# Performance work log

Measured on AMD Instinct MI355X. Metric: run time of the kernel, lower is better.

The kernel has to match this reference:

```python
import jax, jax.numpy as jnp
import numpy as np

B, T, D, H = 2, 2048, 1024, 16
DH = D // H
EPS = 1e-5


def layer_norm(x, g, b):
    m = jnp.mean(x, axis=-1, keepdims=True)
    v = jnp.mean((x - m) ** 2, axis=-1, keepdims=True)
    return (x - m) * jax.lax.rsqrt(v + EPS) * g + b


def setup_inputs() -> dict:
    key = jax.random.key(0)
    ks = jax.random.split(key, 12)
    s = 0.02
    return {
        "x_refined": jax.random.normal(ks[0], (B, T, D), jnp.float32),
        "x_mem": jax.random.normal(ks[1], (B, T, D), jnp.float32),
        "ln_q_g": jnp.ones((D,), jnp.float32), "ln_q_b": jnp.zeros((D,), jnp.float32),
        "ln_kv_g": jnp.ones((D,), jnp.float32), "ln_kv_b": jnp.zeros((D,), jnp.float32),
        "Wq": jax.random.normal(ks[2], (D, D), jnp.float32) * s,
        "bq": jnp.zeros((D,), jnp.float32),
        "Wk": jax.random.normal(ks[3], (D, D), jnp.float32) * s,
        "bk": jnp.zeros((D,), jnp.float32),
        "Wv": jax.random.normal(ks[4], (D, D), jnp.float32) * s,
        "bv": jnp.zeros((D,), jnp.float32),
        "Wo": jax.random.normal(ks[5], (D, D), jnp.float32) * s,
        "bo": jnp.zeros((D,), jnp.float32),
        "ln_f_g": jnp.ones((D,), jnp.float32), "ln_f_b": jnp.zeros((D,), jnp.float32),
        "W1": jax.random.normal(ks[6], (D, 4 * D), jnp.float32) * s,
        "b1": jnp.zeros((4 * D,), jnp.float32),
        "W2": jax.random.normal(ks[7], (4 * D, D), jnp.float32) * s,
        "b2": jnp.zeros((D,), jnp.float32),
        "band": 24,
    }


def reference(x_refined, x_mem, ln_q_g, ln_q_b, ln_kv_g, ln_kv_b,
              Wq, bq, Wk, bk, Wv, bv, Wo, bo,
              ln_f_g, ln_f_b, W1, b1, W2, b2, band):
    Q = layer_norm(x_refined, ln_q_g, ln_q_b)   # (B,T,D)
    KV = layer_norm(x_mem, ln_kv_g, ln_kv_b)    # (B,T,D)

    # projections, split into heads: (B,H,T,DH)
    q = (Q @ Wq + bq).reshape(B, T, H, DH).transpose(0, 2, 1, 3)
    k = (KV @ Wk + bk).reshape(B, T, H, DH).transpose(0, 2, 1, 3)
    v = (KV @ Wv + bv).reshape(B, T, H, DH).transpose(0, 2, 1, 3)

    scores = jnp.einsum('bhtd,bhsd->bhts', q, k) / jnp.sqrt(jnp.float32(DH))
    # banded additive mask: |t - s| <= band allowed (same math as the Python loop)
    idx = jnp.arange(T)
    allowed = jnp.abs(idx[:, None] - idx[None, :]) <= band  # (T,T)
    scores = jnp.where(allowed[None, None], scores, -jnp.inf)
    attn = jax.nn.softmax(scores, axis=-1)

    ctx = jnp.einsum('bhts,bhsd->bhtd', attn, v)            # (B,H,T,DH)
    ctx = ctx.transpose(0, 2, 1, 3).reshape(B, T, D)
    y = x_refined + (ctx @ Wo + bo)

    h = layer_norm(y, ln_f_g, ln_f_b)
    h = jax.nn.gelu(h @ W1 + b1, approximate=False) @ W2 + b2
    return y + h
```

## Files before the change

kernel.cpp:

```cpp
#include <hip/hip_runtime.h>
#include <math.h>
#include <stdint.h>

#define TSEQ   2048
#define DMODEL 1024
#define NHEAD  16
#define DHEAD  64
#define MROWS  4096

typedef short bf16x8 __attribute__((ext_vector_type(8)));
typedef float f32x4  __attribute__((ext_vector_type(4)));
typedef unsigned short u16;

typedef __attribute__((address_space(3))) unsigned int lds_u32_t;
typedef __attribute__((address_space(1))) unsigned int glb_u32_t;

static __device__ __forceinline__ u16 f2bf(float f) {
    unsigned u = __float_as_uint(f);
    u += 0x7FFFu + ((u >> 16) & 1u);
    return (u16)(u >> 16);
}
static __device__ __forceinline__ float bf2f(u16 h) {
    return __uint_as_float(((unsigned)h) << 16);
}

__global__ __launch_bounds__(256) void tc_kernel(
    const float* __restrict__ W, u16* __restrict__ Wt, int K, int N)
{
    __shared__ u16 tile[32][33];
    const int n0 = blockIdx.x * 32, k0 = blockIdx.y * 32;
    const int t = threadIdx.x;
    const int tx = t & 31, ty = t >> 5;
#pragma unroll
    for (int i = 0; i < 4; ++i) {
        int kk = ty + i * 8;
        tile[kk][tx] = f2bf(W[(size_t)(k0 + kk) * N + n0 + tx]);
    }
    __syncthreads();
#pragma unroll
    for (int i = 0; i < 4; ++i) {
        int nn = ty + i * 8;
        Wt[(size_t)(n0 + nn) * K + k0 + tx] = tile[tx][nn];
    }
}

__global__ __launch_bounds__(256) void biaspack_kernel(
    const float* __restrict__ bq, const float* __restrict__ bk,
    const float* __restrict__ bv, float* __restrict__ o)
{
    const int i = blockIdx.x * 256 + threadIdx.x;
    if (i < 1024) o[i] = bq[i];
    else if (i < 2048) o[i] = bk[i - 1024];
    else if (i < 3072) o[i] = bv[i - 2048];
}

__global__ __launch_bounds__(256) void vt_kernel(
    const u16* __restrict__ qkv, u16* __restrict__ vT)
{
    __shared__ __align__(16) u16 tile[64][72];
    const int bb = blockIdx.z;
    const int t0 = blockIdx.x * 64;
    const int c0 = blockIdx.y * 64;
    const int tid = threadIdx.x;
    const int r = tid >> 2;
    const int c = (tid & 3) * 16;
    const u16* src = qkv + (size_t)(bb * TSEQ + t0 + r) * 3072 + 2048 + c0 + c;
    *(bf16x8*)&tile[r][c]     = *(const bf16x8*)(src);
    *(bf16x8*)&tile[r][c + 8] = *(const bf16x8*)(src + 8);
    __syncthreads();
    u16 o[16];
#pragma unroll
    for (int j = 0; j < 16; ++j) o[j] = tile[c + j][r];
    u16* dst = vT + (size_t)(bb * 1024 + c0 + r) * TSEQ + t0 + c;
    *(bf16x8*)dst       = *(bf16x8*)&o[0];
    *(bf16x8*)(dst + 8) = *(bf16x8*)&o[8];
}

__global__ __launch_bounds__(256) void ln_kernel(
    const float* __restrict__ x, const float* __restrict__ g,
    const float* __restrict__ b, u16* __restrict__ out)
{
    const int row = blockIdx.x;
    const int t = threadIdx.x;
    const float4 v = ((const float4*)(x + (size_t)row * DMODEL))[t];
    float s  = v.x + v.y + v.z + v.w;
    float s2 = v.x * v.x + v.y * v.y + v.z * v.z + v.w * v.w;
#pragma unroll
    for (int m = 32; m >= 1; m >>= 1) { s += __shfl_xor(s, m); s2 += __shfl_xor(s2, m); }
    __shared__ float ps[4], ps2[4];
    if ((t & 63) == 0) { ps[t >> 6] = s; ps2[t >> 6] = s2; }
    __syncthreads();
    const float S  = ps[0] + ps[1] + ps[2] + ps[3];
    const float S2 = ps2[0] + ps2[1] + ps2[2] + ps2[3];
    const float mean = S * (1.0f / DMODEL);
    const float var  = S2 * (1.0f / DMODEL) - mean * mean;
    const float rstd = rsqrtf(var + 1e-5f);
    const float4 gg = ((const float4*)g)[t];
    const float4 bb = ((const float4*)b)[t];
    u16 o[4];
    o[0] = f2bf((v.x - mean) * rstd * gg.x + bb.x);
    o[1] = f2bf((v.y - mean) * rstd * gg.y + bb.y);
    o[2] = f2bf((v.z - mean) * rstd * gg.z + bb.z);
    o[3] = f2bf((v.w - mean) * rstd * gg.w + bb.w);
    *(short4*)(out + (size_t)row * DMODEL + t * 4) = *(short4*)o;
}

template <int EPI>
__global__ __launch_bounds__(256) void gemm_bt(
    const u16* __restrict__ A, const u16* __restrict__ A2,
    const u16* __restrict__ Wt,
    const float* __restrict__ bias, const float* __restrict__ resid,
    u16* __restrict__ Cb, float* __restrict__ Cf, float* __restrict__ Cf2,
    int M, int N, int K, int kl, int gx)
{
    __shared__ __align__(16) u16 As[128 * 32];
    __shared__ __align__(16) u16 Bs[128 * 32];

    const int nwg = gridDim.x;
    const int bid = blockIdx.x;
    const int swz = (bid & 7) * (nwg >> 3) + (bid >> 3);
    const int bx = swz % gx, by = swz / gx;
    const int m0 = by * 128, n0 = bx * 128;
    const int kofs = blockIdx.y * kl;

    const int t = threadIdx.x;
    const int lane = t & 63;
    const int wv = t >> 6;
    const int wr = wv >> 1, wc = wv & 1;

    const u16* Ause = (A2 != nullptr && n0 >= 1024) ? A2 : A;

    const int strow = t >> 2;
    const int stcol = (t & 3) * 8;
    const u16* gA  = Ause + (size_t)(m0 + strow) * K + kofs + stcol;
    const u16* gA2 = gA + (size_t)64 * K;
    const u16* gB  = Wt + (size_t)(n0 + strow) * K + kofs + stcol;
    const u16* gB2 = gB + (size_t)64 * K;
    char* lA  = (char*)As + wv * 1024;
    char* lA2 = (char*)As + 4096 + wv * 1024;
    char* lB  = (char*)Bs + wv * 1024;
    char* lB2 = (char*)Bs + 4096 + wv * 1024;

    f32x4 zero = {0.f, 0.f, 0.f, 0.f};
    f32x4 acc[4][4];
#pragma unroll
    for (int mi = 0; mi < 4; ++mi)
#pragma unroll
        for (int ni = 0; ni < 4; ++ni) acc[mi][ni] = zero;

    const int fr = lane & 15, fq = lane >> 4;
    const int nk = kl >> 5;
    for (int kt = 0; kt < nk; ++kt) {
        const int k0 = kt << 5;
        __builtin_amdgcn_global_load_lds((const glb_u32_t*)(gA  + k0), (lds_u32_t*)lA,  16, 0, 0);
        __builtin_amdgcn_global_load_lds((const glb_u32_t*)(gA2 + k0), (lds_u32_t*)lA2, 16, 0, 0);
        __builtin_amdgcn_global_load_lds((const glb_u32_t*)(gB  + k0), (lds_u32_t*)lB,  16, 0, 0);
        __builtin_amdgcn_global_load_lds((const glb_u32_t*)(gB2 + k0), (lds_u32_t*)lB2, 16, 0, 0);
        __syncthreads();

        bf16x8 af[4], bfr[4];
#pragma unroll
        for (int mi = 0; mi < 4; ++mi)
            af[mi] = *(const bf16x8*)&As[(wr * 64 + mi * 16 + fr) * 32 + fq * 8];
#pragma unroll
        for (int ni = 0; ni < 4; ++ni)
            bfr[ni] = *(const bf16x8*)&Bs[(wc * 64 + ni * 16 + fr) * 32 + fq * 8];
#pragma unroll
        for (int mi = 0; mi < 4; ++mi)
#pragma unroll
            for (int ni = 0; ni < 4; ++ni)
                acc[mi][ni] = __builtin_amdgcn_mfma_f32_16x16x32_bf16(af[mi], bfr[ni], acc[mi][ni], 0, 0, 0);
        __syncthreads();
    }

    float* Cpart = (EPI == 3) ? (blockIdx.y ? Cf2 : Cf) : Cf;
#pragma unroll
    for (int ni = 0; ni < 4; ++ni) {
        const int col = n0 + wc * 64 + ni * 16 + fr;
        const float bv = (EPI == 3) ? 0.f : bias[col];
#pragma unroll
        for (int mi = 0; mi < 4; ++mi) {
#pragma unroll
            for (int j = 0; j < 4; ++j) {
                const int row = m0 + wr * 64 + mi * 16 + fq * 4 + j;
                float val = acc[mi][ni][j] + bv;
                if (EPI == 1)
                    val = 0.5f * val * (1.0f + erff(val * 0.70710678118654752f));
                if (EPI == 2)
                    Cf[(size_t)row * N + col] = val + resid[(size_t)row * N + col];
                else if (EPI == 3)
                    Cpart[(size_t)row * N + col] = val;
                else
                    Cb[(size_t)row * N + col] = f2bf(val);
            }
        }
    }
}

__global__ __launch_bounds__(256) void redk_kernel(
    const float* __restrict__ p0, const float* __restrict__ p1,
    const float* __restrict__ bias, const float* __restrict__ resid,
    float* __restrict__ out, int n4, int ncols)
{
    const int stride = gridDim.x * 256;
    for (int i = blockIdx.x * 256 + threadIdx.x; i < n4; i += stride) {
        const float4 a = ((const float4*)p0)[i];
        const float4 b = ((const float4*)p1)[i];
        const float4 r = ((const float4*)resid)[i];
        const float4 bb = *(const float4*)&bias[(i * 4) & (ncols - 1)];
        float4 o;
        o.x = a.x + b.x + bb.x + r.x;
        o.y = a.y + b.y + bb.y + r.y;
        o.z = a.z + b.z + bb.z + r.z;
        o.w = a.w + b.w + bb.w + r.w;
        ((float4*)out)[i] = o;
    }
}

__global__ __launch_bounds__(256) void battn_kernel(
    const u16* __restrict__ qkv, const u16* __restrict__ vT,
    u16* __restrict__ ctx, const int* __restrict__ band_ptr)
{
    __shared__ __align__(16) u16 P[4][16][104];
    const int band = *band_ptr;
    const int bid = blockIdx.x;
    const int tile = bid & 31;
    const int h = (bid >> 5) & 15;
    const int b = bid >> 9;
    const int w = threadIdx.x >> 6;
    const int lane = threadIdx.x & 63;
    const int fr = lane & 15, fq = lane >> 4;
    const int t0 = tile * 64 + w * 16;

    const size_t qbase = ((size_t)b * TSEQ) * 3072 + h * DHEAD;
    const size_t kbase = qbase + 1024;
    const size_t cbase = ((size_t)b * TSEQ) * DMODEL + h * DHEAD;

    const bf16x8 aq0 = *(const bf16x8*)&qkv[qbase + (size_t)(t0 + fr) * 3072 + fq * 8];
    const bf16x8 aq1 = *(const bf16x8*)&qkv[qbase + (size_t)(t0 + fr) * 3072 + 32 + fq * 8];

    const int kb0 = t0 - 32;
    const f32x4 zero = {0.f, 0.f, 0.f, 0.f};

    f32x4 sc[5];
#pragma unroll
    for (int kt = 0; kt < 5; ++kt) {
        const int srow = kb0 + kt * 16 + fr;
        const int scl = min(max(srow, 0), TSEQ - 1);
        const bf16x8 kf0 = *(const bf16x8*)&qkv[kbase + (size_t)scl * 3072 + fq * 8];
        const bf16x8 kf1 = *(const bf16x8*)&qkv[kbase + (size_t)scl * 3072 + 32 + fq * 8];
        f32x4 a = zero;
        a = __builtin_amdgcn_mfma_f32_16x16x32_bf16(aq0, kf0, a, 0, 0, 0);
        a = __builtin_amdgcn_mfma_f32_16x16x32_bf16(aq1, kf1, a, 0, 0, 0);
        sc[kt] = a;
    }

    float mx[4], l[4];
#pragma unroll
    for (int j = 0; j < 4; ++j) mx[j] = -1e30f;
#pragma unroll
    for (int kt = 0; kt < 5; ++kt) {
        const int s = kb0 + kt * 16 + fr;
#pragma unroll
        for (int j = 0; j < 4; ++j) {
            const int tq = t0 + fq * 4 + j;
            const bool ok = (s >= 0) && (s < TSEQ) && (abs(tq - s) <= band);
            const float vv = ok ? sc[kt][j] * 0.125f : -1e30f;
            sc[kt][j] = vv;
            mx[j] = fmaxf(mx[j], vv);
        }
    }
#pragma unroll
    for (int m = 1; m <= 8; m <<= 1)
#pragma unroll
        for (int j = 0; j < 4; ++j) mx[j] = fmaxf(mx[j], __shfl_xor(mx[j], m));

#pragma unroll
    for (int j = 0; j < 4; ++j) l[j] = 0.f;
#pragma unroll
    for (int kt = 0; kt < 5; ++kt)
#pragma unroll
        for (int j = 0; j < 4; ++j) {
            const float p = __expf(sc[kt][j] - mx[j]);
            sc[kt][j] = p;
            l[j] += p;
        }
#pragma unroll
    for (int m = 1; m <= 8; m <<= 1)
#pragma unroll
        for (int j = 0; j < 4; ++j) l[j] += __shfl_xor(l[j], m);

#pragma unroll
    for (int kt = 0; kt < 5; ++kt)
#pragma unroll
        for (int j = 0; j < 4; ++j)
            P[w][fq * 4 + j][kt * 16 + fr] = f2bf(sc[kt][j]);
    {
        const short4 z4 = {0, 0, 0, 0};
        *(short4*)&P[w][fr][80 + fq * 4] = z4;
    }
    __syncthreads();

    bf16x8 pa[3];
#pragma unroll
    for (int c = 0; c < 3; ++c)
        pa[c] = *(const bf16x8*)&P[w][fr][c * 32 + fq * 8];

    const size_t vbase = ((size_t)(b * NHEAD + h) * DHEAD) * TSEQ;
    f32x4 cacc[4];
#pragma unroll
    for (int dt = 0; dt < 4; ++dt) cacc[dt] = zero;
#pragma unroll
    for (int dt = 0; dt < 4; ++dt) {
#pragma unroll
        for (int c = 0; c < 3; ++c) {
            const int s8 = kb0 + c * 32 + fq * 8;
            const int s8c = min(max(s8, 0), TSEQ - 8);
            const bf16x8 vf = *(const bf16x8*)&vT[vbase + (size_t)(dt * 16 + fr) * TSEQ + s8c];
            cacc[dt] = __builtin_amdgcn_mfma_f32_16x16x32_bf16(pa[c], vf, cacc[dt], 0, 0, 0);
        }
    }

    float rl[4];
#pragma unroll
    for (int j = 0; j < 4; ++j) rl[j] = 1.0f / l[j];
#pragma unroll
    for (int dt = 0; dt < 4; ++dt)
#pragma unroll
        for (int j = 0; j < 4; ++j)
            ctx[cbase + (size_t)(t0 + fq * 4 + j) * DMODEL + dt * 16 + fr] =
                f2bf(cacc[dt][j] * rl[j]);
}

extern "C" void kernel_launch(void* const* d_in, const int* in_sizes, int n_in,
                              void* d_out, int out_size, void* d_ws, size_t ws_size,
                              hipStream_t stream) {
    const float* x_ref  = (const float*)d_in[0];
    const float* x_mem  = (const float*)d_in[1];
    const float* ln_q_g = (const float*)d_in[2];
    const float* ln_q_b = (const float*)d_in[3];
    const float* ln_kv_g= (const float*)d_in[4];
    const float* ln_kv_b= (const float*)d_in[5];
    const float* Wq = (const float*)d_in[6];
    const float* bq = (const float*)d_in[7];
    const float* Wk = (const float*)d_in[8];
    const float* bk = (const float*)d_in[9];
    const float* Wv = (const float*)d_in[10];
    const float* bv = (const float*)d_in[11];
    const float* Wo = (const float*)d_in[12];
    const float* bo = (const float*)d_in[13];
    const float* ln_f_g = (const float*)d_in[14];
    const float* ln_f_b = (const float*)d_in[15];
    const float* W1 = (const float*)d_in[16];
    const float* b1 = (const float*)d_in[17];
    const float* W2 = (const float*)d_in[18];
    const float* b2 = (const float*)d_in[19];
    const int*  band = (const int*)d_in[20];
    float* out = (float*)d_out;

    char* ws = (char*)d_ws;
    const size_t MB = 1024 * 1024;
    if (ws_size < 128 * MB) return;
    u16*   wt_qkv = (u16*)(ws + 0 * MB);
    u16*   wt_o   = (u16*)(ws + 6 * MB);
    u16*   wt_1   = (u16*)(ws + 8 * MB);
    u16*   wt_2   = (u16*)(ws + 16 * MB);
    float* bqkv   = (float*)(ws + 24 * MB);
    u16*   aq     = (u16*)(ws + 25 * MB);
    u16*   akv    = (u16*)(ws + 33 * MB);
    u16*   qkvb   = (u16*)(ws + 41 * MB);
    u16*   vTb    = (u16*)(ws + 65 * MB);
    u16*   ctxb   = (u16*)(ws + 73 * MB);
    float* y      = (float*)(ws + 81 * MB);
    u16*   hb     = (u16*)(ws + 97 * MB);
    u16*   a1     = (u16*)(ws + 25 * MB);
    float* p0     = (float*)(ws + 57 * MB);
    float* p1     = (float*)(ws + 97 * MB);

    dim3 blk(256);
    tc_kernel<<<dim3(32, 32),  blk, 0, stream>>>(Wq, wt_qkv,               1024, 1024);
    tc_kernel<<<dim3(32, 32),  blk, 0, stream>>>(Wk, wt_qkv + 1024 * 1024, 1024, 1024);
    tc_kernel<<<dim3(32, 32),  blk, 0, stream>>>(Wv, wt_qkv + 2048 * 1024, 1024, 1024);
    tc_kernel<<<dim3(32, 32),  blk, 0, stream>>>(Wo, wt_o, 1024, 1024);
    tc_kernel<<<dim3(128, 32), blk, 0, stream>>>(W1, wt_1, 1024, 4096);
    tc_kernel<<<dim3(32, 128), blk, 0, stream>>>(W2, wt_2, 4096, 1024);
    biaspack_kernel<<<12, blk, 0, stream>>>(bq, bk, bv, bqkv);
    ln_kernel<<<MROWS, blk, 0, stream>>>(x_ref, ln_q_g, ln_q_b, aq);
    ln_kernel<<<MROWS, blk, 0, stream>>>(x_mem, ln_kv_g, ln_kv_b, akv);
    gemm_bt<0><<<dim3(768), blk, 0, stream>>>(aq, akv, wt_qkv, bqkv, nullptr,
                                              qkvb, nullptr, nullptr,
                                              MROWS, 3072, 1024, 1024, 24);
    vt_kernel<<<dim3(32, 16, 2), blk, 0, stream>>>(qkvb, vTb);
    battn_kernel<<<1024, blk, 0, stream>>>(qkvb, vTb, ctxb, band);
    gemm_bt<2><<<dim3(256), blk, 0, stream>>>(ctxb, nullptr, wt_o, bo, x_ref,
                                              nullptr, y, nullptr,
                                              MROWS, 1024, 1024, 1024, 8);
    ln_kernel<<<MROWS, blk, 0, stream>>>(y, ln_f_g, ln_f_b, hb);
    gemm_bt<1><<<dim3(1024), blk, 0, stream>>>(hb, nullptr, wt_1, b1, nullptr,
                                               a1, nullptr, nullptr,
                                               MROWS, 4096, 1024, 1024, 32);
    gemm_bt<3><<<dim3(256, 2), blk, 0, stream>>>(a1, nullptr, wt_2, nullptr, nullptr,
                                                 nullptr, p0, p1,
                                                 MROWS, 1024, 4096, 2048, 8);
    redk_kernel<<<2048, blk, 0, stream>>>(p0, p1, b2, y, out, MROWS * 1024 / 4, 1024);
}
```

Measured before the change: 408.2 us.

## Double-buffer GEMM LDS loads, remap tiles per XCD, stage bf16 epilogue through LDS

```diff
diff --git a/kernel.cpp b/kernel.cpp
--- a/kernel.cpp
+++ b/kernel.cpp
@@ -10,6 +10,7 @@
 
 typedef short bf16x8 __attribute__((ext_vector_type(8)));
 typedef float f32x4  __attribute__((ext_vector_type(4)));
+typedef uint64_t u64x2 __attribute__((ext_vector_type(2)));
 typedef unsigned short u16;
 
 typedef __attribute__((address_space(3))) unsigned int lds_u32_t;
@@ -111,16 +112,18 @@
     const u16* __restrict__ Wt,
     const float* __restrict__ bias, const float* __restrict__ resid,
     u16* __restrict__ Cb, float* __restrict__ Cf, float* __restrict__ Cf2,
-    int M, int N, int K, int kl, int gx)
-{
-    __shared__ __align__(16) u16 As[128 * 32];
-    __shared__ __align__(16) u16 Bs[128 * 32];
-
-    const int nwg = gridDim.x;
+    int N, int K, int kl, int gx, int cx)
+{
+    extern __shared__ __align__(16) char smem[];
+
     const int bid = blockIdx.x;
-    const int swz = (bid & 7) * (nwg >> 3) + (bid >> 3);
-    const int bx = swz % gx, by = swz / gx;
-    const int m0 = by * 128, n0 = bx * 128;
+    const int xcd = bid & 7, jj = bid >> 3;
+    const int sx = gx / cx;
+    const int sy = (gridDim.x >> 3) / sx;
+    const int xr = xcd / cx, xc = xcd % cx;
+    const int jr = jj / sx, jc = jj % sx;
+    const int m0 = (xr * sy + jr) * 128;
+    const int n0 = (xc * sx + jc) * 128;
     const int kofs = blockIdx.y * kl;
 
     const int t = threadIdx.x;
@@ -136,10 +139,14 @@
     const u16* gA2 = gA + (size_t)64 * K;
     const u16* gB  = Wt + (size_t)(n0 + strow) * K + kofs + stcol;
     const u16* gB2 = gB + (size_t)64 * K;
-    char* lA  = (char*)As + wv * 1024;
-    char* lA2 = (char*)As + 4096 + wv * 1024;
-    char* lB  = (char*)Bs + wv * 1024;
-    char* lB2 = (char*)Bs + 4096 + wv * 1024;
+
+#define STAGE(bufi, k0) do {                                                            \
+    char* _b = smem + (bufi) * 16384 + wv * 1024;                                       \
+    __builtin_amdgcn_global_load_lds((const glb_u32_t*)(gA  + (k0)), (lds_u32_t*)(_b),          16, 0, 0); \
+    __builtin_amdgcn_global_load_lds((const glb_u32_t*)(gA2 + (k0)), (lds_u32_t*)(_b + 4096),  16, 0, 0); \
+    __builtin_amdgcn_global_load_lds((const glb_u32_t*)(gB  + (k0)), (lds_u32_t*)(_b + 8192),  16, 0, 0); \
+    __builtin_amdgcn_global_load_lds((const glb_u32_t*)(gB2 + (k0)), (lds_u32_t*)(_b + 12288), 16, 0, 0); \
+} while (0)
 
     f32x4 zero = {0.f, 0.f, 0.f, 0.f};
     f32x4 acc[4][4];
@@ -150,48 +157,84 @@
 
     const int fr = lane & 15, fq = lane >> 4;
     const int nk = kl >> 5;
+
+    STAGE(0, 0);
+    STAGE(1, 32);
+
     for (int kt = 0; kt < nk; ++kt) {
-        const int k0 = kt << 5;
-        __builtin_amdgcn_global_load_lds((const glb_u32_t*)(gA  + k0), (lds_u32_t*)lA,  16, 0, 0);
-        __builtin_amdgcn_global_load_lds((const glb_u32_t*)(gA2 + k0), (lds_u32_t*)lA2, 16, 0, 0);
-        __builtin_amdgcn_global_load_lds((const glb_u32_t*)(gB  + k0), (lds_u32_t*)lB,  16, 0, 0);
-        __builtin_amdgcn_global_load_lds((const glb_u32_t*)(gB2 + k0), (lds_u32_t*)lB2, 16, 0, 0);
-        __syncthreads();
-
+        const int cur = kt & 1;
+        if (kt < nk - 1) { asm volatile("s_waitcnt vmcnt(4)" ::: "memory"); }
+        else             { asm volatile("s_waitcnt vmcnt(0)" ::: "memory"); }
+        __builtin_amdgcn_s_barrier();
+
+        const u16* As_ = (const u16*)smem + cur * 8192;
+        const u16* Bs_ = As_ + 4096;
         bf16x8 af[4], bfr[4];
 #pragma unroll
         for (int mi = 0; mi < 4; ++mi)
-            af[mi] = *(const bf16x8*)&As[(wr * 64 + mi * 16 + fr) * 32 + fq * 8];
+            af[mi] = *(const bf16x8*)&As_[(wr * 64 + mi * 16 + fr) * 32 + fq * 8];
 #pragma unroll
         for (int ni = 0; ni < 4; ++ni)
-            bfr[ni] = *(const bf16x8*)&Bs[(wc * 64 + ni * 16 + fr) * 32 + fq * 8];
+            bfr[ni] = *(const bf16x8*)&Bs_[(wc * 64 + ni * 16 + fr) * 32 + fq * 8];
+
+        __builtin_amdgcn_s_setprio(1);
 #pragma unroll
         for (int mi = 0; mi < 4; ++mi)
 #pragma unroll
             for (int ni = 0; ni < 4; ++ni)
                 acc[mi][ni] = __builtin_amdgcn_mfma_f32_16x16x32_bf16(af[mi], bfr[ni], acc[mi][ni], 0, 0, 0);
+        __builtin_amdgcn_s_setprio(0);
+        __builtin_amdgcn_sched_barrier(0);
+        __builtin_amdgcn_s_barrier();
+        if (kt + 2 < nk) STAGE(cur, (kt + 2) << 5);
+    }
+#undef STAGE
+
+    if (EPI <= 1) {
+        u16* cs = (u16*)smem;
+#pragma unroll
+        for (int ni = 0; ni < 4; ++ni) {
+            const int col = wc * 64 + ni * 16 + fr;
+            const float bv = bias[n0 + col];
+#pragma unroll
+            for (int mi = 0; mi < 4; ++mi) {
+#pragma unroll
+                for (int j = 0; j < 4; ++j) {
+                    const int row = wr * 64 + mi * 16 + fq * 4 + j;
+                    float val = acc[mi][ni][j] + bv;
+                    if (EPI == 1)
+                        val = 0.5f * val * (1.0f + erff(val * 0.70710678118654752f));
+                    cs[row * 132 + col] = f2bf(val);
+                }
+            }
+        }
         __syncthreads();
-    }
-
-    float* Cpart = (EPI == 3) ? (blockIdx.y ? Cf2 : Cf) : Cf;
-#pragma unroll
-    for (int ni = 0; ni < 4; ++ni) {
-        const int col = n0 + wc * 64 + ni * 16 + fr;
-        const float bv = (EPI == 3) ? 0.f : bias[col];
-#pragma unroll
-        for (int mi = 0; mi < 4; ++mi) {
-#pragma unroll
-            for (int j = 0; j < 4; ++j) {
-                const int row = m0 + wr * 64 + mi * 16 + fq * 4 + j;
-                float val = acc[mi][ni][j] + bv;
-                if (EPI == 1)
-                    val = 0.5f * val * (1.0f + erff(val * 0.70710678118654752f));
-                if (EPI == 2)
-                    Cf[(size_t)row * N + col] = val + resid[(size_t)row * N + col];
-                else if (EPI == 3)
-                    Cpart[(size_t)row * N + col] = val;
-                else
-                    Cb[(size_t)row * N + col] = f2bf(val);
+        const int rr = t >> 4, cc = (t & 15) * 8;
+#pragma unroll
+        for (int c8 = 0; c8 < 8; ++c8) {
+            const int row = c8 * 16 + rr;
+            const uint64_t lo = *(const uint64_t*)&cs[row * 132 + cc];
+            const uint64_t hi = *(const uint64_t*)&cs[row * 132 + cc + 4];
+            u64x2 v; v.x = lo; v.y = hi;
+            *(u64x2*)&Cb[(size_t)(m0 + row) * N + n0 + cc] = v;
+        }
+    } else {
+        float* Cpart = (EPI == 3) ? (blockIdx.y ? Cf2 : Cf) : Cf;
+#pragma unroll
+        for (int ni = 0; ni < 4; ++ni) {
+            const int col = n0 + wc * 64 + ni * 16 + fr;
+            const float bv = (EPI == 3) ? 0.f : bias[col];
+#pragma unroll
+            for (int mi = 0; mi < 4; ++mi) {
+#pragma unroll
+                for (int j = 0; j < 4; ++j) {
+                    const int row = m0 + wr * 64 + mi * 16 + fq * 4 + j;
+                    float val = acc[mi][ni][j] + bv;
+                    if (EPI == 2)
+                        Cf[(size_t)row * N + col] = val + resid[(size_t)row * N + col];
+                    else
+                        Cpart[(size_t)row * N + col] = val;
+                }
             }
         }
     }
@@ -378,6 +421,9 @@
     float* p1     = (float*)(ws + 97 * MB);
 
     dim3 blk(256);
+    const size_t SM_GEMM = 32768;
+    const size_t SM_BF16 = 33792;
+
     tc_kernel<<<dim3(32, 32),  blk, 0, stream>>>(Wq, wt_qkv,               1024, 1024);
     tc_kernel<<<dim3(32, 32),  blk, 0, stream>>>(Wk, wt_qkv + 1024 * 1024, 1024, 1024);
     tc_kernel<<<dim3(32, 32),  blk, 0, stream>>>(Wv, wt_qkv + 2048 * 1024, 1024, 1024);
@@ -387,20 +433,20 @@
     biaspack_kernel<<<12, blk, 0, stream>>>(bq, bk, bv, bqkv);
     ln_kernel<<<MROWS, blk, 0, stream>>>(x_ref, ln_q_g, ln_q_b, aq);
     ln_kernel<<<MROWS, blk, 0, stream>>>(x_mem, ln_kv_g, ln_kv_b, akv);
-    gemm_bt<0><<<dim3(768), blk, 0, stream>>>(aq, akv, wt_qkv, bqkv, nullptr,
-                                              qkvb, nullptr, nullptr,
-                                              MROWS, 3072, 1024, 1024, 24);
+    gemm_bt<0><<<dim3(768), blk, SM_BF16, stream>>>(aq, akv, wt_qkv, bqkv, nullptr,
+                                                    qkvb, nullptr, nullptr,
+                                                    3072, 1024, 1024, 24, 2);
     vt_kernel<<<dim3(32, 16, 2), blk, 0, stream>>>(qkvb, vTb);
     battn_kernel<<<1024, blk, 0, stream>>>(qkvb, vTb, ctxb, band);
-    gemm_bt<2><<<dim3(256), blk, 0, stream>>>(ctxb, nullptr, wt_o, bo, x_ref,
-                                              nullptr, y, nullptr,
-                                              MROWS, 1024, 1024, 1024, 8);
+    gemm_bt<2><<<dim3(256), blk, SM_GEMM, stream>>>(ctxb, nullptr, wt_o, bo, x_ref,
+                                                    nullptr, y, nullptr,
+                                                    1024, 1024, 1024, 8, 1);
     ln_kernel<<<MROWS, blk, 0, stream>>>(y, ln_f_g, ln_f_b, hb);
-    gemm_bt<1><<<dim3(1024), blk, 0, stream>>>(hb, nullptr, wt_1, b1, nullptr,
-                                               a1, nullptr, nullptr,
-                                               MROWS, 4096, 1024, 1024, 32);
-    gemm_bt<3><<<dim3(256, 2), blk, 0, stream>>>(a1, nullptr, wt_2, nullptr, nullptr,
-                                                 nullptr, p0, p1,
-                                                 MROWS, 1024, 4096, 2048, 8);
+    gemm_bt<1><<<dim3(1024), blk, SM_BF16, stream>>>(hb, nullptr, wt_1, b1, nullptr,
+                                                     a1, nullptr, nullptr,
+                                                     4096, 1024, 1024, 32, 2);
+    gemm_bt<3><<<dim3(256, 2), blk, SM_GEMM, stream>>>(a1, nullptr, wt_2, nullptr, nullptr,
+                                                       nullptr, p0, p1,
+                                                       1024, 4096, 2048, 8, 1);
     redk_kernel<<<2048, blk, 0, stream>>>(p0, p1, b2, y, out, MROWS * 1024 / 4, 1024);
 }
```

New measurement: 365.6 us. 1.12x faster.
